# Kernel optimization log

Measured on AMD Instinct MI355X. Metric: run time of the kernel, lower is better.

Reference implementation:

```python
import jax, jax.numpy as jnp
import numpy as np


def setup_inputs() -> dict:
    key = jax.random.key(0)
    ks = jax.random.split(key, 6)
    B, S, D, H = 8, 1024, 1024, 16
    dk = D // H
    inputs = jax.random.normal(ks[0], (B, S, D), dtype=jnp.float32)
    mask = jnp.ones((B, S), dtype=jnp.float32)
    scale = 0.02
    W_q = jax.random.normal(ks[1], (H, D, dk), dtype=jnp.float32) * scale
    W_k = jax.random.normal(ks[2], (H, D, dk), dtype=jnp.float32) * scale
    W_v = jax.random.normal(ks[3], (D, D), dtype=jnp.float32) * scale
    W_o = jax.random.normal(ks[4], (D, D), dtype=jnp.float32) * scale
    return {"inputs": inputs, "mask": mask, "W_q": W_q, "W_k": W_k,
            "W_v": W_v, "W_o": W_o}


def reference(inputs, mask, W_q, W_k, W_v, W_o):
    B, S, D = inputs.shape
    H, _, dk = W_q.shape
    # combined causal + padding mask: 1.0 where attention is disallowed
    causal = 1.0 - jnp.tril(jnp.ones((S, S), dtype=jnp.float32))  # [S,S]
    input_mask = mask[:, None, :] * mask[:, :, None]              # [B,S,S]
    bad = jnp.maximum(causal[None, :, :], 1.0 - input_mask)       # [B,S,S]

    V = jnp.einsum('bsd,de->bse', inputs, W_v)                    # shared values
    Q = jnp.einsum('bsd,hdk->bhsk', inputs, W_q)
    K = jnp.einsum('bsd,hdk->bhsk', inputs, W_k)
    scores = jnp.einsum('bhqk,bhsk->bhqs', Q, K) / jnp.sqrt(jnp.float32(dk))
    scores = scores - bad[:, None, :, :] * 1e9
    attn = jax.nn.softmax(scores, axis=-1)                        # [B,H,S,S]
    attn_avg = jnp.mean(attn, axis=1)                             # [B,S,S]
    Hout = jnp.einsum('bqs,bse->bqe', attn_avg, V)
    output = jnp.einsum('bqe,ed->bqd', Hout, W_o)
    return (output, attn_avg)
```

## Files before the change

kernel.cpp:

```cpp
#include <hip/hip_runtime.h>

typedef unsigned short ushort;
typedef __bf16 bf16x8 __attribute__((ext_vector_type(8)));
typedef float f32x4 __attribute__((ext_vector_type(4)));
typedef unsigned short us8v __attribute__((ext_vector_type(8)));

__device__ __forceinline__ ushort f2bf(float f) {
  unsigned u = __builtin_bit_cast(unsigned, f);
  u += 0x7FFFu + ((u >> 16) & 1u);
  return (ushort)(u >> 16);
}

__device__ __forceinline__ bf16x8 ld_bf16x8(const ushort* p) {
  uint4 v = *(const uint4*)p;
  return __builtin_bit_cast(bf16x8, v);
}

__device__ __forceinline__ void gl16(const ushort* g, ushort* l) {
  __builtin_amdgcn_global_load_lds(
      (const __attribute__((address_space(1))) void*)g,
      (__attribute__((address_space(3))) void*)l, 16, 0, 0);
}

__global__ __launch_bounds__(256) void pack_x(const float* __restrict__ in,
                                              ushort* __restrict__ out) {
  long i = (long)blockIdx.x * 256 + threadIdx.x;
  const float4* s = (const float4*)in;
  float4 a = s[i * 2], b = s[i * 2 + 1];
  us8v o;
  o[0] = f2bf(a.x); o[1] = f2bf(a.y); o[2] = f2bf(a.z); o[3] = f2bf(a.w);
  o[4] = f2bf(b.x); o[5] = f2bf(b.y); o[6] = f2bf(b.z); o[7] = f2bf(b.w);
  *(us8v*)&out[i * 8] = o;
}

__global__ __launch_bounds__(256) void transpose_pack(
    const float* __restrict__ src, ushort* __restrict__ dst,
    int sC, int dLd, long sBatch, long dBatch, float scale) {
  src += (long)blockIdx.z * sBatch;
  dst += (long)blockIdx.z * dBatch;
  const int r0 = blockIdx.y * 64, c0 = blockIdx.x * 64;
  __shared__ ushort T[64 * 68];
  const int t = threadIdx.x;
#pragma unroll
  for (int i = 0; i < 4; ++i) {
    int ch = t + 256 * i;
    int r = ch >> 4, c4 = ch & 15;
    float4 v = *(const float4*)&src[(long)(r0 + r) * sC + c0 + c4 * 4];
    T[(c4 * 4 + 0) * 68 + r] = f2bf(v.x * scale);
    T[(c4 * 4 + 1) * 68 + r] = f2bf(v.y * scale);
    T[(c4 * 4 + 2) * 68 + r] = f2bf(v.z * scale);
    T[(c4 * 4 + 3) * 68 + r] = f2bf(v.w * scale);
  }
  __syncthreads();
#pragma unroll
  for (int i = 0; i < 4; ++i) {
    int ch = t + 256 * i;
    int c = ch >> 4, r4 = ch & 15;
    ushort4 o;
    o.x = T[c * 68 + r4 * 4 + 0];
    o.y = T[c * 68 + r4 * 4 + 1];
    o.z = T[c * 68 + r4 * 4 + 2];
    o.w = T[c * 68 + r4 * 4 + 3];
    *(ushort4*)&dst[(long)(c0 + c) * dLd + r0 + r4 * 4] = o;
  }
}

template <int EPI, bool CAUSAL, int NWC>
__global__ __launch_bounds__(512, 2) void gemm256(
    const ushort* __restrict__ A, const ushort* __restrict__ Bt,
    int M, int N, int K, long aB, long bB,
    ushort* __restrict__ O_q, ushort* __restrict__ O_k, ushort* __restrict__ O_v,
    ushort* __restrict__ O_b, long oB,
    float* __restrict__ O_f) {
  constexpr int BN = NWC * 64;
  constexpr int WM = 8 / NWC;
  constexpr int MR = 16 / WM;
  __shared__ __align__(16) ushort As[2][256 * 64];
  __shared__ __align__(16) ushort Bs[2][BN * 64];
  const int tid = threadIdx.x;
  const int lane = tid & 63, w = tid >> 6;
  const int lr = lane & 15, lg = lane >> 4;

  const int nx = gridDim.x, ny = gridDim.y;
  long nwg = (long)nx * ny * gridDim.z;
  long hwid = blockIdx.x + (long)nx * (blockIdx.y + (long)ny * blockIdx.z);
  long cpx = nwg >> 3;
  long sid = (hwid & 7) * cpx + (hwid >> 3);
  int bx = (int)(sid % nx);
  int t2 = (int)(sid / nx);
  int by = t2 % ny, z = t2 / ny;

  const int row0 = by * 256, col0 = bx * BN;
  A += (long)z * aB;
  Bt += (long)z * bB;
  const int wrow = (w / NWC) * (MR * 16);
  const int wcol = (w % NWC) * 64;

  f32x4 acc[MR][4] = {};
  const int kmax = CAUSAL ? (K < row0 + 256 ? K : row0 + 256) : K;
  const int nk = kmax >> 6;

  auto stage = [&](int buf, int kt) {
    const int k0 = kt << 6;
#pragma unroll
    for (int j = 0; j < 4; ++j) {
      int c = tid + 512 * j;
      int r = c >> 3, c8 = (c & 7) ^ (r & 7);
      gl16(&A[(long)(row0 + r) * K + k0 + c8 * 8], &As[buf][c * 8]);
    }
#pragma unroll
    for (int j = 0; j < BN / 64; ++j) {
      int c = tid + 512 * j;
      int r = c >> 3, c8 = (c & 7) ^ (r & 7);
      gl16(&Bt[(long)(col0 + r) * K + k0 + c8 * 8], &Bs[buf][c * 8]);
    }
  };
  auto compute = [&](int buf) {
#pragma unroll
    for (int kk = 0; kk < 2; ++kk) {
      bf16x8 af[MR], bfr[4];
#pragma unroll
      for (int m = 0; m < MR; ++m) {
        int row = wrow + m * 16 + lr;
        int c8 = (kk * 4 + lg) ^ (row & 7);
        af[m] = ld_bf16x8(&As[buf][row * 64 + c8 * 8]);
      }
#pragma unroll
      for (int n = 0; n < 4; ++n) {
        int row = wcol + n * 16 + lr;
        int c8 = (kk * 4 + lg) ^ (row & 7);
        bfr[n] = ld_bf16x8(&Bs[buf][row * 64 + c8 * 8]);
      }
#pragma unroll
      for (int m = 0; m < MR; ++m)
#pragma unroll
        for (int n = 0; n < 4; ++n)
          acc[m][n] = __builtin_amdgcn_mfma_f32_16x16x32_bf16(af[m], bfr[n], acc[m][n], 0, 0, 0);
    }
  };

  stage(0, 0);
  __syncthreads();
  for (int kt = 1; kt < nk; ++kt) {
    stage(kt & 1, kt);
    compute((kt - 1) & 1);
    __syncthreads();
  }
  compute((nk - 1) & 1);

#pragma unroll
  for (int m = 0; m < MR; ++m)
#pragma unroll
    for (int n = 0; n < 4; ++n)
#pragma unroll
      for (int r = 0; r < 4; ++r) {
        int gr = row0 + wrow + m * 16 + lg * 4 + r;
        int gc = col0 + wcol + n * 16 + lr;
        float v = acc[m][n][r];
        if (EPI == 0) {
          int b = gr >> 10, s = gr & 1023;
          if (gc < 1024) {
            int h = gc >> 6, kq = gc & 63;
            O_q[(((long)(b * 16 + h) << 10) + s) * 64 + kq] = f2bf(v);
          } else if (gc < 2048) {
            int n2 = gc - 1024;
            int h = n2 >> 6, kq = n2 & 63;
            O_k[(((long)(b * 16 + h) << 10) + s) * 64 + kq] = f2bf(v);
          } else {
            int e = gc - 2048;
            O_v[((long)(b << 10) + e) * 1024 + s] = f2bf(v);
          }
        } else if (EPI == 1) {
          (O_b + (long)z * oB)[(long)gr * N + gc] = f2bf(v);
        } else {
          O_f[(long)gr * N + gc] = v;
        }
      }
}

__global__ __launch_bounds__(512, 2) void attn16(
    const ushort* __restrict__ Qb, const ushort* __restrict__ Kb,
    const float* __restrict__ mask, float* __restrict__ attn_out,
    ushort* __restrict__ attnb) {
  __shared__ __align__(16) ushort Ks[8 * 128 * 64];
  __shared__ float redS[8][16];
  const int tid = threadIdx.x;
  const int lane = tid & 63, w = tid >> 6;
  const int lr = lane & 15, lg = lane >> 4;
  const int hw = blockIdx.x + 64 * blockIdx.y;
  const int b = hw & 7;
  const int idx = hw >> 3;
  const int qt = (idx & 1) ? 63 - (idx >> 1) : (idx >> 1);
  const int q0 = qt * 16;
  const int NT = (qt >> 3) + 1;
  const int NTW = (qt >> 4) * 2 + 2;
  const int nch = NT << 10;

  float mq[4], ms[8];
#pragma unroll
  for (int r = 0; r < 4; ++r) mq[r] = mask[b * 1024 + q0 + lg * 4 + r];
#pragma unroll
  for (int t = 0; t < 8; ++t) ms[t] = mask[b * 1024 + t * 128 + w * 16 + lr];

  {
    const long hb = ((long)(b * 16)) << 10;
#pragma unroll 2
    for (int i = tid; i < nch; i += 512) {
      int st = i >> 10, r = (i >> 3) & 127, c8 = i & 7;
      gl16(&Kb[(hb + st * 128 + r) * 64 + ((c8 ^ (r & 7)) << 3)], &Ks[i * 8]);
    }
  }
  __syncthreads();

  const int row = w * 16 + lr;
  const int cs0 = ((0 + lg) ^ (row & 7)) * 8;
  const int cs1 = ((4 + lg) ^ (row & 7)) * 8;

  f32x4 acc[8] = {};
#pragma unroll 1
  for (int h = 0; h < 16; ++h) {
    const long hb = ((long)(b * 16 + h)) << 10;
    const bf16x8 qf0 = ld_bf16x8(&Qb[(hb + q0 + lr) * 64 + lg * 8]);
    const bf16x8 qf1 = ld_bf16x8(&Qb[(hb + q0 + lr) * 64 + 32 + lg * 8]);
    f32x4 sc[8];
    float ps[4] = {0.f, 0.f, 0.f, 0.f};
#pragma unroll
    for (int t = 0; t < 8; ++t) {
      const int sb = t * 128 + w * 16;
      if (sb <= q0) {
        const ushort* kr = &Ks[t * 8192 + row * 64];
        bf16x8 k0 = ld_bf16x8(kr + cs0);
        bf16x8 k1 = ld_bf16x8(kr + cs1);
        f32x4 d = {};
        d = __builtin_amdgcn_mfma_f32_16x16x32_bf16(qf0, k0, d, 0, 0, 0);
        d = __builtin_amdgcn_mfma_f32_16x16x32_bf16(qf1, k1, d, 0, 0, 0);
#pragma unroll
        for (int r = 0; r < 4; ++r) {
          float e = __expf(d[r]) * (mq[r] * ms[t]);
          if (sb == q0) e = (lr <= lg * 4 + r) ? e : 0.f;
          sc[t][r] = e;
          ps[r] += e;
        }
      }
    }
#pragma unroll
    for (int r = 0; r < 4; ++r) {
      ps[r] += __shfl_xor(ps[r], 1);
      ps[r] += __shfl_xor(ps[r], 2);
      ps[r] += __shfl_xor(ps[r], 4);
      ps[r] += __shfl_xor(ps[r], 8);
    }
    if (lr == 0) {
#pragma unroll
      for (int r = 0; r < 4; ++r) redS[w][lg * 4 + r] = ps[r];
    }
    __syncthreads();

    if (h < 15) {
      const long hb2 = ((long)(b * 16 + h + 1)) << 10;
#pragma unroll 2
      for (int i = tid; i < nch; i += 512) {
        int st = i >> 10, r = (i >> 3) & 127, c8 = i & 7;
        gl16(&Kb[(hb2 + st * 128 + r) * 64 + ((c8 ^ (r & 7)) << 3)], &Ks[i * 8]);
      }
    }

#pragma unroll
    for (int r = 0; r < 4; ++r) {
      float tot = 0.f;
#pragma unroll
      for (int ww = 0; ww < 8; ++ww) tot += redS[ww][lg * 4 + r];
      float rinv = __builtin_amdgcn_rcpf(tot);
#pragma unroll
      for (int t = 0; t < 8; ++t) {
        const int sb = t * 128 + w * 16;
        if (sb <= q0) acc[t][r] += sc[t][r] * rinv;
      }
    }
    if (h < 15) __syncthreads();
  }

#pragma unroll
  for (int t = 0; t < 8; ++t) {
    int s = t * 128 + w * 16 + lr;
#pragma unroll
    for (int r = 0; r < 4; ++r) {
      int q = q0 + lg * 4 + r;
      float v = acc[t][r] * 0.0625f;
      long o = ((long)(b * 1024 + q) << 10) + s;
      attn_out[o] = v;
      if (t < NTW) attnb[o] = f2bf(v);
    }
  }
}

extern "C" void kernel_launch(void* const* d_in, const int* in_sizes, int n_in,
                              void* d_out, int out_size, void* d_ws, size_t ws_size,
                              hipStream_t stream) {
  const float* inputs = (const float*)d_in[0];
  const float* mask   = (const float*)d_in[1];
  const float* W_q    = (const float*)d_in[2];
  const float* W_k    = (const float*)d_in[3];
  const float* W_v    = (const float*)d_in[4];
  const float* W_o    = (const float*)d_in[5];
  float* out = (float*)d_out;

  ushort* Xb    = (ushort*)d_ws;
  ushort* WqkvT = Xb + 8192L * 1024;
  ushort* WoT   = WqkvT + 3072L * 1024;
  ushort* Qb    = WoT + 1024L * 1024;
  ushort* Kb    = Qb + 8L * 16 * 1024 * 64;
  ushort* Vt    = Kb + 8L * 16 * 1024 * 64;
  ushort* attnb = Vt + 8L * 1024 * 1024;
  ushort* Houtb = attnb + 8L * 1024 * 1024;

  pack_x<<<4096, 256, 0, stream>>>(inputs, Xb);
  transpose_pack<<<dim3(1, 16, 16), 256, 0, stream>>>(W_q, WqkvT, 64, 1024,
                                                      65536L, 64L * 1024, 0.125f);
  transpose_pack<<<dim3(1, 16, 16), 256, 0, stream>>>(W_k, WqkvT + 1024L * 1024, 64, 1024,
                                                      65536L, 64L * 1024, 1.0f);
  transpose_pack<<<dim3(16, 16, 1), 256, 0, stream>>>(W_v, WqkvT + 2048L * 1024, 1024, 1024,
                                                      0L, 0L, 1.0f);
  transpose_pack<<<dim3(16, 16, 1), 256, 0, stream>>>(W_o, WoT, 1024, 1024,
                                                      0L, 0L, 1.0f);
  gemm256<0, false, 4><<<dim3(12, 32, 1), 512, 0, stream>>>(
      Xb, WqkvT, 8192, 3072, 1024, 0L, 0L, Qb, Kb, Vt, nullptr, 0L, nullptr);
  attn16<<<dim3(64, 8), 512, 0, stream>>>(Qb, Kb, mask, out + 8388608L, attnb);
  gemm256<1, true, 2><<<dim3(8, 4, 8), 512, 0, stream>>>(
      attnb, Vt, 1024, 1024, 1024, 1048576L, 1048576L,
      nullptr, nullptr, nullptr, Houtb, 1048576L, nullptr);
  gemm256<2, false, 2><<<dim3(8, 32, 1), 512, 0, stream>>>(
      Houtb, WoT, 8192, 1024, 1024, 0L, 0L,
      nullptr, nullptr, nullptr, nullptr, 0L, out);
}
```

Measured before the change: 281.2 us.

## Replace double-buffered GEMM with single-buffer 2x4-wave tiles and BN=192 for QKV

The GEMM kernel drops its double-buffered LDS staging in favour of a single buffer with a barrier before and after each k-tile load. Waves are rearranged into a 2x4 grid, each covering 128 rows, and A fragments are loaded one at a time so fewer registers are live. The QKV projection now uses 192-wide column tiles, which gives 16 column blocks instead of 12. The smaller LDS footprint is meant to let two workgroups share a CU so they hide each other's load latency, in exchange for losing overlap of loads and MFMA work inside one workgroup.

```diff
diff --git a/kernel.cpp b/kernel.cpp
--- a/kernel.cpp
+++ b/kernel.cpp
@@ -65,18 +65,16 @@
   }
 }
 
-template <int EPI, bool CAUSAL, int NWC>
-__global__ __launch_bounds__(512, 2) void gemm256(
+template <int EPI, bool CAUSAL, int BN>
+__global__ __launch_bounds__(512, 2) void gemmS(
     const ushort* __restrict__ A, const ushort* __restrict__ Bt,
-    int M, int N, int K, long aB, long bB,
+    int N, int K, long aB, long bB,
     ushort* __restrict__ O_q, ushort* __restrict__ O_k, ushort* __restrict__ O_v,
     ushort* __restrict__ O_b, long oB,
     float* __restrict__ O_f) {
-  constexpr int BN = NWC * 64;
-  constexpr int WM = 8 / NWC;
-  constexpr int MR = 16 / WM;
-  __shared__ __align__(16) ushort As[2][256 * 64];
-  __shared__ __align__(16) ushort Bs[2][BN * 64];
+  constexpr int NC = BN / 64;
+  __shared__ __align__(16) ushort As[256 * 64];
+  __shared__ __align__(16) ushort Bs[BN * 64];
   const int tid = threadIdx.x;
   const int lane = tid & 63, w = tid >> 6;
   const int lr = lane & 15, lg = lane >> 4;
@@ -93,65 +91,54 @@
   const int row0 = by * 256, col0 = bx * BN;
   A += (long)z * aB;
   Bt += (long)z * bB;
-  const int wrow = (w / NWC) * (MR * 16);
-  const int wcol = (w % NWC) * 64;
-
-  f32x4 acc[MR][4] = {};
+  const int wrow = (w >> 2) * 128;
+  const int wcol = (w & 3) * (BN / 4);
+
+  f32x4 acc[8][NC] = {};
   const int kmax = CAUSAL ? (K < row0 + 256 ? K : row0 + 256) : K;
   const int nk = kmax >> 6;
 
-  auto stage = [&](int buf, int kt) {
+  for (int kt = 0; kt < nk; ++kt) {
     const int k0 = kt << 6;
+    __syncthreads();
 #pragma unroll
     for (int j = 0; j < 4; ++j) {
       int c = tid + 512 * j;
       int r = c >> 3, c8 = (c & 7) ^ (r & 7);
-      gl16(&A[(long)(row0 + r) * K + k0 + c8 * 8], &As[buf][c * 8]);
-    }
-#pragma unroll
-    for (int j = 0; j < BN / 64; ++j) {
+      gl16(&A[(long)(row0 + r) * K + k0 + c8 * 8], &As[c * 8]);
+    }
+#pragma unroll
+    for (int j = 0; j < NC; ++j) {
       int c = tid + 512 * j;
       int r = c >> 3, c8 = (c & 7) ^ (r & 7);
-      gl16(&Bt[(long)(col0 + r) * K + k0 + c8 * 8], &Bs[buf][c * 8]);
-    }
-  };
-  auto compute = [&](int buf) {
+      gl16(&Bt[(long)(col0 + r) * K + k0 + c8 * 8], &Bs[c * 8]);
+    }
+    __syncthreads();
 #pragma unroll
     for (int kk = 0; kk < 2; ++kk) {
-      bf16x8 af[MR], bfr[4];
-#pragma unroll
-      for (int m = 0; m < MR; ++m) {
+      bf16x8 bfr[NC];
+#pragma unroll
+      for (int n = 0; n < NC; ++n) {
+        int row = wcol + n * 16 + lr;
+        int c8 = (kk * 4 + lg) ^ (row & 7);
+        bfr[n] = ld_bf16x8(&Bs[row * 64 + c8 * 8]);
+      }
+#pragma unroll
+      for (int m = 0; m < 8; ++m) {
         int row = wrow + m * 16 + lr;
         int c8 = (kk * 4 + lg) ^ (row & 7);
-        af[m] = ld_bf16x8(&As[buf][row * 64 + c8 * 8]);
-      }
-#pragma unroll
-      for (int n = 0; n < 4; ++n) {
-        int row = wcol + n * 16 + lr;
-        int c8 = (kk * 4 + lg) ^ (row & 7);
-        bfr[n] = ld_bf16x8(&Bs[buf][row * 64 + c8 * 8]);
-      }
-#pragma unroll
-      for (int m = 0; m < MR; ++m)
-#pragma unroll
-        for (int n = 0; n < 4; ++n)
-          acc[m][n] = __builtin_amdgcn_mfma_f32_16x16x32_bf16(af[m], bfr[n], acc[m][n], 0, 0, 0);
-    }
-  };
-
-  stage(0, 0);
-  __syncthreads();
-  for (int kt = 1; kt < nk; ++kt) {
-    stage(kt & 1, kt);
-    compute((kt - 1) & 1);
-    __syncthreads();
-  }
-  compute((nk - 1) & 1);
-
-#pragma unroll
-  for (int m = 0; m < MR; ++m)
-#pragma unroll
-    for (int n = 0; n < 4; ++n)
+        bf16x8 af = ld_bf16x8(&As[row * 64 + c8 * 8]);
+#pragma unroll
+        for (int n = 0; n < NC; ++n)
+          acc[m][n] = __builtin_amdgcn_mfma_f32_16x16x32_bf16(af, bfr[n], acc[m][n], 0, 0, 0);
+      }
+    }
+  }
+
+#pragma unroll
+  for (int m = 0; m < 8; ++m)
+#pragma unroll
+    for (int n = 0; n < NC; ++n)
 #pragma unroll
       for (int r = 0; r < 4; ++r) {
         int gr = row0 + wrow + m * 16 + lg * 4 + r;
@@ -323,13 +310,13 @@
                                                       0L, 0L, 1.0f);
   transpose_pack<<<dim3(16, 16, 1), 256, 0, stream>>>(W_o, WoT, 1024, 1024,
                                                       0L, 0L, 1.0f);
-  gemm256<0, false, 4><<<dim3(12, 32, 1), 512, 0, stream>>>(
-      Xb, WqkvT, 8192, 3072, 1024, 0L, 0L, Qb, Kb, Vt, nullptr, 0L, nullptr);
+  gemmS<0, false, 192><<<dim3(16, 32, 1), 512, 0, stream>>>(
+      Xb, WqkvT, 3072, 1024, 0L, 0L, Qb, Kb, Vt, nullptr, 0L, nullptr);
   attn16<<<dim3(64, 8), 512, 0, stream>>>(Qb, Kb, mask, out + 8388608L, attnb);
-  gemm256<1, true, 2><<<dim3(8, 4, 8), 512, 0, stream>>>(
-      attnb, Vt, 1024, 1024, 1024, 1048576L, 1048576L,
+  gemmS<1, true, 128><<<dim3(8, 4, 8), 512, 0, stream>>>(
+      attnb, Vt, 1024, 1024, 1048576L, 1048576L,
       nullptr, nullptr, nullptr, Houtb, 1048576L, nullptr);
-  gemm256<2, false, 2><<<dim3(8, 32, 1), 512, 0, stream>>>(
-      Houtb, WoT, 8192, 1024, 1024, 0L, 0L,
+  gemmS<2, false, 128><<<dim3(8, 32, 1), 512, 0, stream>>>(
+      Houtb, WoT, 1024, 1024, 0L, 0L,
       nullptr, nullptr, nullptr, nullptr, 0L, out);
 }
```

New measurement: 277.1 us (median of 5 runs). Within noise of the previous version (-1.5%).
